# Kernel optimization log

Measured on AMD Instinct MI355X. Metric: run time of the kernel, lower is better.

## Reference

```python
import jax, jax.numpy as jnp
import numpy as np

IN_DIM = 1024
HID = 256
OUT_DIM = 1000
NUM_BINS = 51
BATCH = 2048
N_LEGAL = 200


def setup_inputs() -> dict:
    key = jax.random.key(0)
    ks = jax.random.split(key, 12)
    s = lambda fan_in: 1.0 / np.sqrt(fan_in)
    u = lambda k, shp, b: jax.random.uniform(k, shp, jnp.float32, -b, b)
    return {
        "x": jax.random.normal(ks[0], (BATCH, IN_DIM), jnp.float32),
        # weights stored as [in, out] (math-equivalent to torch Linear)
        "w_in": u(ks[1], (IN_DIM, HID), s(IN_DIM)),
        "b_in": u(ks[2], (HID,), s(IN_DIM)),
        "w_ah": u(ks[3], (HID, HID), s(HID)),
        "b_ah": u(ks[4], (HID,), s(HID)),
        "w_ao": u(ks[5], (HID, OUT_DIM * NUM_BINS), s(HID)),
        "b_ao": u(ks[6], (OUT_DIM * NUM_BINS,), s(HID)),
        "w_vh": u(ks[7], (HID, HID), s(HID)),
        "b_vh": u(ks[8], (HID,), s(HID)),
        "w_vo": u(ks[9], (HID, NUM_BINS), s(HID)),
        "b_vo": u(ks[10], (NUM_BINS,), s(HID)),
        "v_range": jnp.linspace(-10.0, 10.0, NUM_BINS, dtype=jnp.float32),
        "possible_moves": jax.random.randint(ks[11], (BATCH, N_LEGAL), 0, OUT_DIM),
    }


def reference(x, w_in, b_in, w_ah, b_ah, w_ao, b_ao, w_vh, b_vh, w_vo, b_vo,
              v_range, possible_moves):
    B = x.shape[0]
    h = jax.nn.relu(x @ w_in + b_in)                       # [B, 256]
    adv_h = jax.nn.relu(h @ w_ah + b_ah)                   # [B, 256]
    val_h = jax.nn.relu(h @ w_vh + b_vh)                   # [B, 256]
    adv = (adv_h @ w_ao + b_ao).reshape(B, OUT_DIM, NUM_BINS)
    val = (val_h @ w_vo + b_vo).reshape(B, 1, NUM_BINS)
    q = val + adv - adv.mean(axis=1, keepdims=True)        # [B, A, bins]
    p = jnp.maximum(jax.nn.softmax(q, axis=2), 1e-5)       # softmax + clamp(min=1e-5)
    q_vals = jnp.sum(p * v_range, axis=2)                  # [B, A]
    # LegalSoftmax: per-row scatter of 1.0 at legal indices, vectorized
    mask = jnp.zeros((B, OUT_DIM), x.dtype).at[
        jnp.arange(B)[:, None], possible_moves].set(1.0)
    filtered = q_vals * mask
    # faithful to torch: any exact-zero entry (masked OR coincidental) -> -inf
    return jnp.where(filtered == 0, -jnp.inf, filtered)
```

## Files before the change

### kernel.cpp

```cpp
#include <hip/hip_runtime.h>
#include <cstdint>
#include <cstddef>

#define NB      2048
#define INDIM   1024
#define HID     256
#define NA      1000
#define BINS    51
#define NLEG    200
#define NPAIR   (NB*NLEG)
#define NBLK    256
#define PPB     (NPAIR/NBLK)

#define NEG_SENTINEL (-1.0e30f)

typedef float    f32x4  __attribute__((ext_vector_type(4)));
typedef __bf16   bf16x8 __attribute__((ext_vector_type(8)));
typedef unsigned short us8 __attribute__((ext_vector_type(8)));
typedef unsigned short us4 __attribute__((ext_vector_type(4)));
typedef unsigned long long u64x2 __attribute__((ext_vector_type(2)));

__device__ __forceinline__ unsigned short f2bf(float f) {
  union { float f; unsigned u; } v; v.f = f;
  return (unsigned short)((v.u + 0x7FFFu + ((v.u >> 16) & 1u)) >> 16);
}
__device__ __forceinline__ float bf2f(unsigned short h) {
  union { unsigned u; float f; } v; v.u = ((unsigned)h) << 16;
  return v.f;
}
__device__ __forceinline__ bf16x8 as_bf(us8 v) { return __builtin_bit_cast(bf16x8, v); }
__device__ __forceinline__ int imin(int a, int b) { return a < b ? a : b; }

__device__ __forceinline__ unsigned f2fp8x4(float a, float b, float c, float d) {
  int v = 0;
  v = __builtin_amdgcn_cvt_pk_fp8_f32(a, b, v, false);
  v = __builtin_amdgcn_cvt_pk_fp8_f32(c, d, v, true);
  return (unsigned)v;
}
__device__ __forceinline__ unsigned char f2fp8(float f) {
  int v = __builtin_amdgcn_cvt_pk_fp8_f32(f, 0.f, 0, false);
  return (unsigned char)(v & 0xff);
}
__device__ __forceinline__ float fp82f(unsigned char u) {
  return __builtin_amdgcn_cvt_f32_fp8((int)u, 0);
}

__device__ __forceinline__ void pack_body(
    int s, int a0, char* smem, int tid,
    const float* __restrict__ w_ao, unsigned char* __restrict__ wp8,
    float* __restrict__ wmean_acc) {
  unsigned char* st = (unsigned char*)smem;
  const float* wbase = w_ao + (size_t)(s * 32) * (NA * BINS) + a0 * BINS;
  for (int i = tid; i < 32 * 102; i += 256) {
    int r = i / 102, c4 = i - r * 102;
    float4 f = *(const float4*)(wbase + (size_t)r * (NA * BINS) + c4 * 4);
    *(unsigned*)(st + r * 420 + c4 * 4) =
        f2fp8x4(f.x * 16.f, f.y * 16.f, f.z * 16.f, f.w * 16.f);
  }
  __syncthreads();
  for (int i = tid; i < 32 * 51; i += 256) {
    int r = i / 51, j = i - r * 51;
    float s8 = 0.f;
#pragma unroll
    for (int aL = 0; aL < 8; aL++) s8 += fp82f(st[r * 420 + aL * 51 + j]);
    atomicAdd(&wmean_acc[(size_t)(s * 32 + r) * BINS + j], s8);
  }
  int t4 = (tid >> 6) & 3, l = tid & 63;
  int col = t4 * 16 + (l & 15), kg = l >> 4;
  for (int aL = 0; aL < 8; aL++) {
    unsigned lo = 0, hi = 0;
    if (col < BINS) {
      const unsigned char* p0 = st + (kg * 8) * 420 + aL * 51 + col;
      lo = (unsigned)p0[0] | ((unsigned)p0[420] << 8) |
           ((unsigned)p0[840] << 16) | ((unsigned)p0[1260] << 24);
      hi = (unsigned)p0[1680] | ((unsigned)p0[2100] << 8) |
           ((unsigned)p0[2520] << 16) | ((unsigned)p0[2940] << 24);
    }
    uint2 v; v.x = lo; v.y = hi;
    *(uint2*)(wp8 + (size_t)(a0 + aL) * 16384 +
              (size_t)((s * 2 + (t4 >> 1)) * 64 + l) * 16 + (t4 & 1) * 8) = v;
  }
}

__global__ __launch_bounds__(256) void k_phase1(
    const float* __restrict__ w_ao, unsigned char* __restrict__ wp8,
    float* __restrict__ wmean_acc,
    const float* __restrict__ w_in, const float* __restrict__ w_ah,
    const float* __restrict__ w_vh,
    unsigned short* __restrict__ w_inT, unsigned short* __restrict__ w_ahT,
    unsigned short* __restrict__ w_vhT,
    float* __restrict__ out, const int* __restrict__ pm,
    int* __restrict__ cnt,
    const float* __restrict__ x, unsigned short* __restrict__ x_bf) {
  __shared__ __align__(16) char smem[13440];
  int b = blockIdx.x, tid = threadIdx.x;
  if (b < 500) {
    pack_body(b & 3, (b >> 2) * 8, smem, tid, w_ao, wp8, wmean_acc);
  } else if (b < 884) {
    int bb = b - 500;
    float (*tile)[33] = (float(*)[33])smem;
    const float* w; unsigned short* wT; int K, N, kt, nt;
    if (bb < 256)      { w = w_in; wT = w_inT; K = INDIM; N = HID; kt = bb & 31;        nt = bb >> 5; }
    else if (bb < 320) { w = w_ah; wT = w_ahT; K = HID;   N = HID; kt = (bb - 256) & 7; nt = (bb - 256) >> 3; }
    else               { w = w_vh; wT = w_vhT; K = HID;   N = HID; kt = (bb - 320) & 7; nt = (bb - 320) >> 3; }
    int k0 = kt * 32, n0 = nt * 32;
    int cr = tid >> 5, cc = tid & 31;
#pragma unroll
    for (int it = 0; it < 4; it++)
      tile[cr + it * 8][cc] = w[(size_t)(k0 + cr + it * 8) * N + n0 + cc];
    __syncthreads();
#pragma unroll
    for (int it = 0; it < 4; it++)
      wT[(size_t)(n0 + cr + it * 8) * K + k0 + cc] = f2bf(tile[cc][cr + it * 8]);
  } else if (b < 1384) {
    int base = (b - 884) * 1024 + tid;
    float4 v = {NEG_SENTINEL, NEG_SENTINEL, NEG_SENTINEL, NEG_SENTINEL};
#pragma unroll
    for (int it = 0; it < 4; it++) ((float4*)out)[base + it * 256] = v;
  } else if (b < 1640) {
    int* lh = (int*)smem;
    int blk = b - 1384;
    for (int i = tid; i < NA; i += 256) lh[i] = 0;
    __syncthreads();
    int base = blk * PPB;
    for (int i = tid; i < PPB; i += 256) atomicAdd(&lh[pm[base + i]], 1);
    __syncthreads();
    for (int a = tid; a < NA; a += 256) {
      int v = lh[a];
      if (v) atomicAdd(&cnt[a], v);
    }
  } else {
    int base4 = (b - 1640) * 1024 + tid;
#pragma unroll
    for (int it = 0; it < 4; it++) {
      float4 v = ((const float4*)x)[base4 + it * 256];
      us4 o;
      o[0] = f2bf(v.x); o[1] = f2bf(v.y); o[2] = f2bf(v.z); o[3] = f2bf(v.w);
      ((us4*)x_bf)[base4 + it * 256] = o;
    }
  }
}

__global__ __launch_bounds__(256) void k_phase2(
    const float* __restrict__ w_ao, unsigned char* __restrict__ wp8,
    float* __restrict__ wmean_acc,
    const int* __restrict__ cnt,
    const unsigned short* __restrict__ x_bf, const unsigned short* __restrict__ w_inT,
    const float* __restrict__ b_in, unsigned short* __restrict__ h_bf,
    int* __restrict__ off, int* __restrict__ cursor) {
  __shared__ __align__(16) char smem[13440];
  int b = blockIdx.x, tid = threadIdx.x;
  if (b < 500) {
    pack_body(4 + (b & 3), (b >> 2) * 8, smem, tid, w_ao, wp8, wmean_acc);
  } else if (b < 1012) {
    int w = tid >> 6, l = tid & 63, la = l & 15, g = l >> 4;
    int idx = (b - 500) * 4 + w;
    int m0 = (idx & 127) * 16, n0 = (idx >> 7) * 16;
    f32x4 acc = {0.f, 0.f, 0.f, 0.f};
    const us8* Bp = (const us8*)(w_inT + (size_t)(n0 + la) * INDIM) + g;
    const us8* Ap = (const us8*)(x_bf + (size_t)(m0 + la) * INDIM) + g;
#pragma unroll 8
    for (int s = 0; s < 32; s++)
      acc = __builtin_amdgcn_mfma_f32_16x16x32_bf16(as_bf(Ap[s * 4]), as_bf(Bp[s * 4]),
                                                    acc, 0, 0, 0);
    float bb = b_in[n0 + la];
#pragma unroll
    for (int r = 0; r < 4; r++) {
      float v = fmaxf(acc[r] + bb, 0.f);
      h_bf[(size_t)(m0 + g * 4 + r) * HID + n0 + la] = f2bf(v);
    }
  } else {
    int* s = (int*)smem;
    int t = tid, i0 = 4 * t;
    int v0 = (i0     < NA) ? cnt[i0]     : 0;
    int v1 = (i0 + 1 < NA) ? cnt[i0 + 1] : 0;
    int v2 = (i0 + 2 < NA) ? cnt[i0 + 2] : 0;
    int v3 = (i0 + 3 < NA) ? cnt[i0 + 3] : 0;
    int sum = v0 + v1 + v2 + v3;
    s[t] = sum;
    __syncthreads();
    for (int d = 1; d < 256; d <<= 1) {
      int u = (t >= d) ? s[t - d] : 0;
      __syncthreads();
      s[t] += u;
      __syncthreads();
    }
    int excl = s[t] - sum;
    if (i0     < NA) { off[i0]     = excl;                cursor[i0]     = excl; }
    if (i0 + 1 < NA) { off[i0 + 1] = excl + v0;           cursor[i0 + 1] = excl + v0; }
    if (i0 + 2 < NA) { off[i0 + 2] = excl + v0 + v1;      cursor[i0 + 2] = excl + v0 + v1; }
    if (i0 + 3 < NA) { off[i0 + 3] = excl + v0 + v1 + v2; cursor[i0 + 3] = excl + v0 + v1 + v2; }
  }
}

__global__ __launch_bounds__(256) void k_phase3(
    const unsigned short* __restrict__ h,
    const unsigned short* __restrict__ wA, const float* __restrict__ bA,
    unsigned char* __restrict__ Aext8, unsigned short* __restrict__ advh_bf,
    const unsigned short* __restrict__ wV, const float* __restrict__ bV,
    unsigned short* __restrict__ oV,
    const int* __restrict__ pm, int* __restrict__ cursor,
    int* __restrict__ rows,
    const float* __restrict__ w_vo, const float* __restrict__ wmean_acc,
    const float* __restrict__ b_vo, const float* __restrict__ b_ao,
    unsigned short* __restrict__ Wc, float* __restrict__ bias_c) {
  __shared__ int lc[NA];
  __shared__ int lbase[NA];
  __shared__ float sred[256];
  int b = blockIdx.x, tid = threadIdx.x;
  if (b < 1024) {
    int w = tid >> 6, l = tid & 63, la = l & 15, g = l >> 4;
    int idx = b * 4 + w;
    int m0 = (idx & 127) * 16;
    int ny = idx >> 7;
    int second = ny >> 4;
    int n0 = (ny & 15) * 16;
    const unsigned short* BT = second ? wV : wA;
    const float* bias = second ? bV : bA;
    f32x4 acc = {0.f, 0.f, 0.f, 0.f};
    const us8* Bp = (const us8*)(BT + (size_t)(n0 + la) * HID) + g;
    const us8* Ap = (const us8*)(h + (size_t)(m0 + la) * HID) + g;
#pragma unroll
    for (int s = 0; s < 8; s++)
      acc = __builtin_amdgcn_mfma_f32_16x16x32_bf16(as_bf(Ap[s * 4]), as_bf(Bp[s * 4]),
                                                    acc, 0, 0, 0);
    float bb = bias[n0 + la];
#pragma unroll
    for (int r = 0; r < 4; r++) {
      float v = fmaxf(acc[r] + bb, 0.f);
      size_t o = (size_t)(m0 + g * 4 + r) * HID + n0 + la;
      if (second) {
        oV[o] = f2bf(v);
      } else {
        advh_bf[o] = f2bf(v);
        Aext8[o] = f2fp8(v);
      }
    }
  } else if (b < 1280) {
    int blk = b - 1024, t = tid;
    for (int i = t; i < NA; i += 256) lc[i] = 0;
    __syncthreads();
    int pbase = blk * PPB;
    for (int i = t; i < PPB; i += 256) atomicAdd(&lc[pm[pbase + i]], 1);
    __syncthreads();
    for (int i = t; i < NA; i += 256) {
      int v = lc[i];
      lbase[i] = v ? atomicAdd(&cursor[i], v) : 0;
      lc[i] = 0;
    }
    __syncthreads();
    for (int i = t; i < PPB; i += 256) {
      int a = pm[pbase + i];
      int r = atomicAdd(&lc[a], 1);
      rows[lbase[a] + r] = (pbase + i) / NLEG;
    }
  } else {
    int n = b - 1280, t = tid;
    for (int k = t; k < 512; k += 256) {
      float v = 0.f;
      if (n < BINS)
        v = (k < 256) ? w_vo[(size_t)k * BINS + n]
                      : (-(0.001f / 16.f) * wmean_acc[(size_t)(k - 256) * BINS + n]);
      Wc[(size_t)n * 512 + k] = f2bf(v);
    }
    float acc = 0.f;
    if (n < BINS)
      for (int a = t; a < NA; a += 256) acc += b_ao[(size_t)a * BINS + n];
    sred[t] = acc;
    __syncthreads();
    for (int d = 128; d > 0; d >>= 1) { if (t < d) sred[t] += sred[t + d]; __syncthreads(); }
    if (t == 0) bias_c[n] = (n < BINS) ? (b_vo[n] - 0.001f * sred[0]) : 0.f;
  }
}

__global__ __launch_bounds__(256) void k_phase4(
    const unsigned short* __restrict__ valh, const unsigned short* __restrict__ advh,
    const unsigned short* __restrict__ Wc, const float* __restrict__ bias_c,
    float* __restrict__ cbuf_f) {
  int b = blockIdx.x, tid = threadIdx.x;
  int w = tid >> 6, l = tid & 63, la = l & 15, g = l >> 4;
  int idx = b * 4 + w;
  int m0 = (idx & 127) * 16;
  int n0 = ((idx >> 7) & 3) * 16;
  int half = idx >> 9;
  const unsigned short* A = half ? advh : valh;
  f32x4 acc = {0.f, 0.f, 0.f, 0.f};
  const us8* Bp = (const us8*)(Wc + (size_t)(n0 + la) * 512 + half * 256) + g;
  const us8* Ap = (const us8*)(A + (size_t)(m0 + la) * HID) + g;
#pragma unroll
  for (int s = 0; s < 8; s++)
    acc = __builtin_amdgcn_mfma_f32_16x16x32_bf16(as_bf(Ap[s * 4]), as_bf(Bp[s * 4]),
                                                  acc, 0, 0, 0);
  float bb = half ? 0.f : bias_c[n0 + la];
#pragma unroll
  for (int r = 0; r < 4; r++)
    atomicAdd(&cbuf_f[(size_t)(m0 + g * 4 + r) * 64 + n0 + la], acc[r] + bb);
}

#define TILE_BODY(TILE, RA_) do {                                              \
  int rA = (RA_);                                                              \
  const long long* Ap = (const long long*)(Aext8 + (size_t)rA * HID) + g;      \
  const float4* cf = (const float4*)(cbuf_f + (size_t)rA * 64);                \
  long long a8[8];                                                             \
  _Pragma("unroll") for (int s = 0; s < 8; s++) a8[s] = Ap[s * 4];             \
  float4 cq0 = cf[g], cq1 = cf[4 + g], cq2 = cf[8 + g], cq3 = cf[12 + g];      \
  f32x4 acc0 = {0.f,0.f,0.f,0.f}, acc1 = {0.f,0.f,0.f,0.f};                    \
  f32x4 acc2 = {0.f,0.f,0.f,0.f}, acc3 = {0.f,0.f,0.f,0.f};                    \
  __builtin_amdgcn_s_setprio(1);                                               \
  _Pragma("unroll") for (int s = 0; s < 8; s++) {                              \
    u64x2 b01 = sBv[(s * 2) * 64 + l];                                         \
    u64x2 b23 = sBv[(s * 2 + 1) * 64 + l];                                     \
    acc0 = __builtin_amdgcn_mfma_f32_16x16x32_fp8_fp8(                         \
        (long long)b01[0], a8[s], acc0, 0, 0, 0);                              \
    acc1 = __builtin_amdgcn_mfma_f32_16x16x32_fp8_fp8(                         \
        (long long)b01[1], a8[s], acc1, 0, 0, 0);                              \
    acc2 = __builtin_amdgcn_mfma_f32_16x16x32_fp8_fp8(                         \
        (long long)b23[0], a8[s], acc2, 0, 0, 0);                              \
    acc3 = __builtin_amdgcn_mfma_f32_16x16x32_fp8_fp8(                         \
        (long long)b23[1], a8[s], acc3, 0, 0, 0);                              \
  }                                                                            \
  __builtin_amdgcn_s_setprio(0);                                               \
  float S = 0.f;                                                               \
  f32x4 e0, e1, e2, e3;                                                        \
  _Pragma("unroll") for (int r = 0; r < 4; r++) {                              \
    e0[r] = __expf(fmaf(acc0[r], 0.0625f, cq0[r] + bao0[r])); S += e0[r];      \
    e1[r] = __expf(fmaf(acc1[r], 0.0625f, cq1[r] + bao1[r])); S += e1[r];      \
    e2[r] = __expf(fmaf(acc2[r], 0.0625f, cq2[r] + bao2[r])); S += e2[r];      \
    e3[r] = __expf(fmaf(acc3[r], 0.0625f, cq3[r] + bao3[r])); S += e3[r];      \
  }                                                                            \
  S += __shfl_xor(S, 16); S += __shfl_xor(S, 32);                              \
  float inv = 1.f / S, qv = 0.f;                                               \
  _Pragma("unroll") for (int r = 0; r < 4; r++) {                              \
    int bin = g * 4 + r;                                                       \
    qv = fmaf(fmaxf(e0[r] * inv, 1e-5f), (float)bin * 0.4f - 10.f, qv);        \
    qv = fmaf(fmaxf(e1[r] * inv, 1e-5f), (float)(bin + 16) * 0.4f - 10.f, qv); \
    qv = fmaf(fmaxf(e2[r] * inv, 1e-5f), (float)(bin + 32) * 0.4f - 10.f, qv); \
    if (bin + 48 < BINS)                                                       \
      qv = fmaf(fmaxf(e3[r] * inv, 1e-5f), (float)(bin + 48) * 0.4f - 10.f, qv); \
  }                                                                            \
  qv += __shfl_xor(qv, 16); qv += __shfl_xor(qv, 32);                          \
  int gi = (TILE) * 16 + la;                                                   \
  if (g == 0 && gi < count)                                                    \
    out[(size_t)rA * NA + a] = (qv == 0.f) ? NEG_SENTINEL : qv;                \
} while (0)

__global__ __launch_bounds__(256) void k_main_mfma(
    const unsigned char* __restrict__ Aext8,
    const float* __restrict__ cbuf_f,
    const unsigned char* __restrict__ wp8,
    const float* __restrict__ b_ao,
    const int* __restrict__ cnt, const int* __restrict__ off,
    const int* __restrict__ rows,
    float* __restrict__ out) {
  __shared__ __align__(16) long long sB8[2048];
  const u64x2* sBv = (const u64x2*)sB8;
  int bx = blockIdx.x;
  int a = (bx & 7) * 125 + (bx >> 3);
  int count = cnt[a];
  int ntiles = (count + 15) >> 4;
  if ((int)(blockIdx.y * 4) >= ntiles) return;
  int tid = threadIdx.x;
  int w = tid >> 6, l = tid & 63, la = l & 15, g = l >> 4;
  int base = off[a];
  int t0 = blockIdx.y * 4 + w;

  int rAq0 = rows[base + imin( t0       * 16 + la, count - 1)];
  int rAq1 = rows[base + imin((t0 +  8) * 16 + la, count - 1)];
  int rAq2 = rows[base + imin((t0 + 16) * 16 + la, count - 1)];
  int rAq3 = rows[base + imin((t0 + 24) * 16 + la, count - 1)];

  const float* baop = b_ao + (size_t)a * BINS;
  f32x4 bao0, bao1, bao2, bao3;
#pragma unroll
  for (int r = 0; r < 4; r++) {
    int bin = g * 4 + r;
    bao0[r] = baop[bin];
    bao1[r] = baop[bin + 16];
    bao2[r] = baop[bin + 32];
    bao3[r] = (bin + 48 < BINS) ? baop[bin + 48] : NEG_SENTINEL;
  }

  const u64x2* wpa = (const u64x2*)(wp8 + (size_t)a * 16384);
#pragma unroll
  for (int i = 0; i < 4; i++) ((u64x2*)sB8)[tid + i * 256] = wpa[tid + i * 256];
  __syncthreads();

  if (t0      < ntiles) TILE_BODY(t0,      rAq0);
  if (t0 +  8 < ntiles) TILE_BODY(t0 +  8, rAq1);
  if (t0 + 16 < ntiles) TILE_BODY(t0 + 16, rAq2);
  if (t0 + 24 < ntiles) TILE_BODY(t0 + 24, rAq3);
  for (int tile = t0 + 32; tile < ntiles; tile += 8) {
    int rAt = rows[base + imin(tile * 16 + la, count - 1)];
    TILE_BODY(tile, rAt);
  }
}

extern "C" void kernel_launch(void* const* d_in, const int* in_sizes, int n_in,
                              void* d_out, int out_size, void* d_ws, size_t ws_size,
                              hipStream_t stream) {
  (void)in_sizes; (void)n_in; (void)out_size; (void)ws_size;
  const float* x     = (const float*)d_in[0];
  const float* w_in  = (const float*)d_in[1];
  const float* b_in  = (const float*)d_in[2];
  const float* w_ah  = (const float*)d_in[3];
  const float* b_ah  = (const float*)d_in[4];
  const float* w_ao  = (const float*)d_in[5];
  const float* b_ao  = (const float*)d_in[6];
  const float* w_vh  = (const float*)d_in[7];
  const float* b_vh  = (const float*)d_in[8];
  const float* w_vo  = (const float*)d_in[9];
  const float* b_vo  = (const float*)d_in[10];
  const int*   pm    = (const int*)d_in[12];
  float* out = (float*)d_out;

  char* p = (char*)d_ws;
  unsigned char*  wp8     = (unsigned char*)p;  p += (size_t)NA * 32 * 512;
  unsigned char*  Aext8   = (unsigned char*)p;  p += (size_t)NB * HID;
  unsigned short* h_bf    = (unsigned short*)p; p += (size_t)NB * HID * 2;
  unsigned short* advh_bf = (unsigned short*)p; p += (size_t)NB * HID * 2;
  unsigned short* valh_bf = (unsigned short*)p; p += (size_t)NB * HID * 2;
  unsigned short* w_inT   = (unsigned short*)p; p += (size_t)HID * INDIM * 2;
  unsigned short* w_ahT   = (unsigned short*)p; p += (size_t)HID * HID * 2;
  unsigned short* w_vhT   = (unsigned short*)p; p += (size_t)HID * HID * 2;
  unsigned short* Wc      = (unsigned short*)p; p += (size_t)64 * 512 * 2;
  unsigned short* x_bf    = (unsigned short*)p; p += (size_t)NB * INDIM * 2;
  float* bias_c = (float*)p; p += 64 * 4;
  float* cbuf_f = (float*)p; p += (size_t)NB * 64 * 4;
  float* wmean  = (float*)p; p += 13056 * 4;
  int* cnt    = (int*)p; p += NA * 4;
  int* off    = (int*)p; p += NA * 4;
  int* cursor = (int*)p; p += (size_t)NA * 4 + 240;
  int* rows   = (int*)p; p += (size_t)NPAIR * 4 + 256;

  hipMemsetAsync(cbuf_f, 0, ((size_t)NB * 64 + 13056 + NA) * sizeof(float), stream);

  k_phase1<<<2152, 256, 0, stream>>>(w_ao, wp8, wmean, w_in, w_ah, w_vh,
                                     w_inT, w_ahT, w_vhT, out, pm, cnt,
                                     x, x_bf);
  k_phase2<<<1013, 256, 0, stream>>>(w_ao, wp8, wmean, cnt,
                                     x_bf, w_inT, b_in, h_bf, off, cursor);
  k_phase3<<<1344, 256, 0, stream>>>(h_bf, w_ahT, b_ah, Aext8, advh_bf,
                                     w_vhT, b_vh, valh_bf, pm, cursor, rows,
                                     w_vo, wmean, b_vo, b_ao, Wc, bias_c);
  k_phase4<<<256, 256, 0, stream>>>(valh_bf, advh_bf, Wc, bias_c, cbuf_f);
  k_main_mfma<<<dim3(1000, 2), 256, 0, stream>>>(Aext8, cbuf_f, wp8, b_ao,
                                                 cnt, off, rows, out);
}
```

Measured before the change: 209.7 us.

## Restructure pipeline into four kernels with fused heads and transposed fp8 packing

After: 209.6 us. No clear change (-0.0%).

```diff
diff --git a/kernel.cpp b/kernel.cpp
--- a/kernel.cpp
+++ b/kernel.cpp
@@ -24,10 +24,6 @@
   union { float f; unsigned u; } v; v.f = f;
   return (unsigned short)((v.u + 0x7FFFu + ((v.u >> 16) & 1u)) >> 16);
 }
-__device__ __forceinline__ float bf2f(unsigned short h) {
-  union { unsigned u; float f; } v; v.u = ((unsigned)h) << 16;
-  return v.f;
-}
 __device__ __forceinline__ bf16x8 as_bf(us8 v) { return __builtin_bit_cast(bf16x8, v); }
 __device__ __forceinline__ int imin(int a, int b) { return a < b ? a : b; }
 
@@ -45,44 +41,7 @@
   return __builtin_amdgcn_cvt_f32_fp8((int)u, 0);
 }
 
-__device__ __forceinline__ void pack_body(
-    int s, int a0, char* smem, int tid,
-    const float* __restrict__ w_ao, unsigned char* __restrict__ wp8,
-    float* __restrict__ wmean_acc) {
-  unsigned char* st = (unsigned char*)smem;
-  const float* wbase = w_ao + (size_t)(s * 32) * (NA * BINS) + a0 * BINS;
-  for (int i = tid; i < 32 * 102; i += 256) {
-    int r = i / 102, c4 = i - r * 102;
-    float4 f = *(const float4*)(wbase + (size_t)r * (NA * BINS) + c4 * 4);
-    *(unsigned*)(st + r * 420 + c4 * 4) =
-        f2fp8x4(f.x * 16.f, f.y * 16.f, f.z * 16.f, f.w * 16.f);
-  }
-  __syncthreads();
-  for (int i = tid; i < 32 * 51; i += 256) {
-    int r = i / 51, j = i - r * 51;
-    float s8 = 0.f;
-#pragma unroll
-    for (int aL = 0; aL < 8; aL++) s8 += fp82f(st[r * 420 + aL * 51 + j]);
-    atomicAdd(&wmean_acc[(size_t)(s * 32 + r) * BINS + j], s8);
-  }
-  int t4 = (tid >> 6) & 3, l = tid & 63;
-  int col = t4 * 16 + (l & 15), kg = l >> 4;
-  for (int aL = 0; aL < 8; aL++) {
-    unsigned lo = 0, hi = 0;
-    if (col < BINS) {
-      const unsigned char* p0 = st + (kg * 8) * 420 + aL * 51 + col;
-      lo = (unsigned)p0[0] | ((unsigned)p0[420] << 8) |
-           ((unsigned)p0[840] << 16) | ((unsigned)p0[1260] << 24);
-      hi = (unsigned)p0[1680] | ((unsigned)p0[2100] << 8) |
-           ((unsigned)p0[2520] << 16) | ((unsigned)p0[2940] << 24);
-    }
-    uint2 v; v.x = lo; v.y = hi;
-    *(uint2*)(wp8 + (size_t)(a0 + aL) * 16384 +
-              (size_t)((s * 2 + (t4 >> 1)) * 64 + l) * 16 + (t4 & 1) * 8) = v;
-  }
-}
-
-__global__ __launch_bounds__(256) void k_phase1(
+__global__ __launch_bounds__(256) void k_pre(
     const float* __restrict__ w_ao, unsigned char* __restrict__ wp8,
     float* __restrict__ wmean_acc,
     const float* __restrict__ w_in, const float* __restrict__ w_ah,
@@ -92,12 +51,67 @@
     float* __restrict__ out, const int* __restrict__ pm,
     int* __restrict__ cnt,
     const float* __restrict__ x, unsigned short* __restrict__ x_bf) {
-  __shared__ __align__(16) char smem[13440];
+  __shared__ __align__(16) unsigned char smem[16320];
   int b = blockIdx.x, tid = threadIdx.x;
-  if (b < 500) {
-    pack_body(b & 3, (b >> 2) * 8, smem, tid, w_ao, wp8, wmean_acc);
-  } else if (b < 884) {
-    int bb = b - 500;
+  if (b < 1000) {
+    unsigned char* st = smem;
+    int s = b & 7, a0 = (b >> 3) * 8;
+    const float* wbase = w_ao + (size_t)(s * 32) * (NA * BINS) + a0 * BINS;
+    for (int i = tid; i < 816; i += 256) {
+      int kq = i / 102, c4 = i - kq * 102;
+      const float* rp = wbase + (size_t)(kq * 4) * (NA * BINS) + c4 * 4;
+      float4 f0 = *(const float4*)(rp);
+      float4 f1 = *(const float4*)(rp + NA * BINS);
+      float4 f2 = *(const float4*)(rp + 2 * NA * BINS);
+      float4 f3 = *(const float4*)(rp + 3 * NA * BINS);
+      unsigned pk0 = f2fp8x4(f0.x * 16.f, f0.y * 16.f, f0.z * 16.f, f0.w * 16.f);
+      unsigned pk1 = f2fp8x4(f1.x * 16.f, f1.y * 16.f, f1.z * 16.f, f1.w * 16.f);
+      unsigned pk2 = f2fp8x4(f2.x * 16.f, f2.y * 16.f, f2.z * 16.f, f2.w * 16.f);
+      unsigned pk3 = f2fp8x4(f3.x * 16.f, f3.y * 16.f, f3.z * 16.f, f3.w * 16.f);
+      unsigned s01lo = __builtin_amdgcn_perm(pk1, pk0, 0x05010400u);
+      unsigned s01hi = __builtin_amdgcn_perm(pk1, pk0, 0x07030602u);
+      unsigned s23lo = __builtin_amdgcn_perm(pk3, pk2, 0x05010400u);
+      unsigned s23hi = __builtin_amdgcn_perm(pk3, pk2, 0x07030602u);
+      unsigned o0 = __builtin_amdgcn_perm(s23lo, s01lo, 0x05040100u);
+      unsigned o1 = __builtin_amdgcn_perm(s23lo, s01lo, 0x07060302u);
+      unsigned o2 = __builtin_amdgcn_perm(s23hi, s01hi, 0x05040100u);
+      unsigned o3 = __builtin_amdgcn_perm(s23hi, s01hi, 0x07060302u);
+      int k4 = kq * 4;
+      int swz = ((c4 >> 2) & 3) << 3;
+      int kb = ((k4 & 24) ^ swz) + (k4 & 7);
+      int cbase = c4 * 160;
+      *(unsigned*)(st + cbase + kb)       = o0;
+      *(unsigned*)(st + cbase + 40 + kb)  = o1;
+      *(unsigned*)(st + cbase + 80 + kb)  = o2;
+      *(unsigned*)(st + cbase + 120 + kb) = o3;
+    }
+    __syncthreads();
+    for (int i = tid; i < 32 * 51; i += 256) {
+      int r = i / 51, j = i - r * 51;
+      float s8 = 0.f;
+#pragma unroll
+      for (int aL = 0; aL < 8; aL++) {
+        int c = aL * 51 + j;
+        s8 += fp82f(st[c * 40 + ((r & 24) ^ (((c >> 4) & 3) << 3)) + (r & 7)]);
+      }
+      atomicAdd(&wmean_acc[(size_t)(s * 32 + r) * BINS + j], s8);
+    }
+    int t4 = (tid >> 6) & 3, l = tid & 63;
+    int col = t4 * 16 + (l & 15), kg = l >> 4;
+    for (int aL = 0; aL < 8; aL++) {
+      unsigned lo = 0, hi = 0;
+      if (col < BINS) {
+        int ci = aL * 51 + col;
+        unsigned long long v8 = *(const unsigned long long*)(
+            st + ci * 40 + ((kg * 8) ^ (((ci >> 4) & 3) << 3)));
+        lo = (unsigned)v8; hi = (unsigned)(v8 >> 32);
+      }
+      uint2 v; v.x = lo; v.y = hi;
+      *(uint2*)(wp8 + (size_t)(a0 + aL) * 16384 +
+                (size_t)((s * 2 + (t4 >> 1)) * 64 + l) * 16 + (t4 & 1) * 8) = v;
+    }
+  } else if (b < 1384) {
+    int bb = b - 1000;
     float (*tile)[33] = (float(*)[33])smem;
     const float* w; unsigned short* wT; int K, N, kt, nt;
     if (bb < 256)      { w = w_in; wT = w_inT; K = INDIM; N = HID; kt = bb & 31;        nt = bb >> 5; }
@@ -112,25 +126,13 @@
 #pragma unroll
     for (int it = 0; it < 4; it++)
       wT[(size_t)(n0 + cr + it * 8) * K + k0 + cc] = f2bf(tile[cc][cr + it * 8]);
-  } else if (b < 1384) {
-    int base = (b - 884) * 1024 + tid;
+  } else if (b < 1884) {
+    int base = (b - 1384) * 1024 + tid;
     float4 v = {NEG_SENTINEL, NEG_SENTINEL, NEG_SENTINEL, NEG_SENTINEL};
 #pragma unroll
     for (int it = 0; it < 4; it++) ((float4*)out)[base + it * 256] = v;
-  } else if (b < 1640) {
-    int* lh = (int*)smem;
-    int blk = b - 1384;
-    for (int i = tid; i < NA; i += 256) lh[i] = 0;
-    __syncthreads();
-    int base = blk * PPB;
-    for (int i = tid; i < PPB; i += 256) atomicAdd(&lh[pm[base + i]], 1);
-    __syncthreads();
-    for (int a = tid; a < NA; a += 256) {
-      int v = lh[a];
-      if (v) atomicAdd(&cnt[a], v);
-    }
-  } else {
-    int base4 = (b - 1640) * 1024 + tid;
+  } else if (b < 2396) {
+    int base4 = (b - 1884) * 1024 + tid;
 #pragma unroll
     for (int it = 0; it < 4; it++) {
       float4 v = ((const float4*)x)[base4 + it * 256];
@@ -138,23 +140,33 @@
       o[0] = f2bf(v.x); o[1] = f2bf(v.y); o[2] = f2bf(v.z); o[3] = f2bf(v.w);
       ((us4*)x_bf)[base4 + it * 256] = o;
     }
+  } else {
+    int* lh = (int*)smem;
+    int blk = b - 2396;
+    for (int i = tid; i < NA; i += 256) lh[i] = 0;
+    __syncthreads();
+    int base = blk * PPB;
+    for (int i = tid; i < PPB; i += 256) atomicAdd(&lh[pm[base + i]], 1);
+    __syncthreads();
+    for (int a = tid; a < NA; a += 256) {
+      int v = lh[a];
+      if (v) atomicAdd(&cnt[a], v);
+    }
   }
 }
 
-__global__ __launch_bounds__(256) void k_phase2(
-    const float* __restrict__ w_ao, unsigned char* __restrict__ wp8,
-    float* __restrict__ wmean_acc,
-    const int* __restrict__ cnt,
+__global__ __launch_bounds__(256) void k_mid(
     const unsigned short* __restrict__ x_bf, const unsigned short* __restrict__ w_inT,
     const float* __restrict__ b_in, unsigned short* __restrict__ h_bf,
-    int* __restrict__ off, int* __restrict__ cursor) {
-  __shared__ __align__(16) char smem[13440];
+    const float* __restrict__ w_vo, const float* __restrict__ wmean_acc,
+    const float* __restrict__ b_vo, const float* __restrict__ b_ao,
+    unsigned short* __restrict__ Wc, float* __restrict__ bias_c,
+    const int* __restrict__ cnt, int* __restrict__ off, int* __restrict__ cursor) {
+  __shared__ __align__(16) char smem[1024];
   int b = blockIdx.x, tid = threadIdx.x;
-  if (b < 500) {
-    pack_body(4 + (b & 3), (b >> 2) * 8, smem, tid, w_ao, wp8, wmean_acc);
-  } else if (b < 1012) {
+  if (b < 512) {
     int w = tid >> 6, l = tid & 63, la = l & 15, g = l >> 4;
-    int idx = (b - 500) * 4 + w;
+    int idx = b * 4 + w;
     int m0 = (idx & 127) * 16, n0 = (idx >> 7) * 16;
     f32x4 acc = {0.f, 0.f, 0.f, 0.f};
     const us8* Bp = (const us8*)(w_inT + (size_t)(n0 + la) * INDIM) + g;
@@ -169,6 +181,23 @@
       float v = fmaxf(acc[r] + bb, 0.f);
       h_bf[(size_t)(m0 + g * 4 + r) * HID + n0 + la] = f2bf(v);
     }
+  } else if (b < 576) {
+    float* sred = (float*)smem;
+    int n = b - 512, t = tid;
+    for (int k = t; k < 512; k += 256) {
+      float v = 0.f;
+      if (n < BINS)
+        v = (k < 256) ? w_vo[(size_t)k * BINS + n]
+                      : (-(0.001f / 16.f) * wmean_acc[(size_t)(k - 256) * BINS + n]);
+      Wc[(size_t)n * 512 + k] = f2bf(v);
+    }
+    float acc = 0.f;
+    if (n < BINS)
+      for (int a = t; a < NA; a += 256) acc += b_ao[(size_t)a * BINS + n];
+    sred[t] = acc;
+    __syncthreads();
+    for (int d = 128; d > 0; d >>= 1) { if (t < d) sred[t] += sred[t + d]; __syncthreads(); }
+    if (t == 0) bias_c[n] = (n < BINS) ? (b_vo[n] - 0.001f * sred[0]) : 0.f;
   } else {
     int* s = (int*)smem;
     int t = tid, i0 = 4 * t;
@@ -193,51 +222,71 @@
   }
 }
 
-__global__ __launch_bounds__(256) void k_phase3(
+__global__ __launch_bounds__(256) void k_heads(
     const unsigned short* __restrict__ h,
     const unsigned short* __restrict__ wA, const float* __restrict__ bA,
-    unsigned char* __restrict__ Aext8, unsigned short* __restrict__ advh_bf,
     const unsigned short* __restrict__ wV, const float* __restrict__ bV,
-    unsigned short* __restrict__ oV,
-    const int* __restrict__ pm, int* __restrict__ cursor,
-    int* __restrict__ rows,
-    const float* __restrict__ w_vo, const float* __restrict__ wmean_acc,
-    const float* __restrict__ b_vo, const float* __restrict__ b_ao,
-    unsigned short* __restrict__ Wc, float* __restrict__ bias_c) {
-  __shared__ int lc[NA];
-  __shared__ int lbase[NA];
-  __shared__ float sred[256];
+    const unsigned short* __restrict__ Wc, const float* __restrict__ bias_c,
+    unsigned char* __restrict__ Aext8, float* __restrict__ cbuf_f,
+    const int* __restrict__ pm, int* __restrict__ cursor, int* __restrict__ rows) {
+  __shared__ __align__(16) char smem[16896];
   int b = blockIdx.x, tid = threadIdx.x;
-  if (b < 1024) {
+  if (b < 128) {
+    unsigned short* aL = (unsigned short*)smem;
+    unsigned short* vL = (unsigned short*)smem + 16 * 264;
     int w = tid >> 6, l = tid & 63, la = l & 15, g = l >> 4;
-    int idx = b * 4 + w;
-    int m0 = (idx & 127) * 16;
-    int ny = idx >> 7;
-    int second = ny >> 4;
-    int n0 = (ny & 15) * 16;
-    const unsigned short* BT = second ? wV : wA;
-    const float* bias = second ? bV : bA;
+    int m0 = b * 16;
+    const us8* Ap = (const us8*)(h + (size_t)(m0 + la) * HID) + g;
+    us8 aF[8];
+#pragma unroll
+    for (int s = 0; s < 8; s++) aF[s] = Ap[s * 4];
+#pragma unroll
+    for (int part = 0; part < 2; part++) {
+      const unsigned short* BT = part ? wV : wA;
+      const float* bias = part ? bV : bA;
+      unsigned short* oL = part ? vL : aL;
+#pragma unroll
+      for (int nt = 0; nt < 4; nt++) {
+        int n0 = w * 64 + nt * 16;
+        f32x4 acc = {0.f, 0.f, 0.f, 0.f};
+        const us8* Bp = (const us8*)(BT + (size_t)(n0 + la) * HID) + g;
+#pragma unroll
+        for (int s = 0; s < 8; s++)
+          acc = __builtin_amdgcn_mfma_f32_16x16x32_bf16(as_bf(aF[s]), as_bf(Bp[s * 4]),
+                                                        acc, 0, 0, 0);
+        float bb = bias[n0 + la];
+#pragma unroll
+        for (int r = 0; r < 4; r++) {
+          float v = fmaxf(acc[r] + bb, 0.f);
+          oL[(g * 4 + r) * 264 + n0 + la] = f2bf(v);
+          if (part == 0)
+            Aext8[(size_t)(m0 + g * 4 + r) * HID + n0 + la] = f2fp8(v);
+        }
+      }
+    }
+    __syncthreads();
+    int n0c = w * 16;
     f32x4 acc = {0.f, 0.f, 0.f, 0.f};
-    const us8* Bp = (const us8*)(BT + (size_t)(n0 + la) * HID) + g;
-    const us8* Ap = (const us8*)(h + (size_t)(m0 + la) * HID) + g;
+    const us8* Vp  = (const us8*)(vL + la * 264) + g;
+    const us8* Ap2 = (const us8*)(aL + la * 264) + g;
+    const us8* BpV = (const us8*)(Wc + (size_t)(n0c + la) * 512) + g;
+    const us8* BpA = (const us8*)(Wc + (size_t)(n0c + la) * 512 + 256) + g;
 #pragma unroll
     for (int s = 0; s < 8; s++)
-      acc = __builtin_amdgcn_mfma_f32_16x16x32_bf16(as_bf(Ap[s * 4]), as_bf(Bp[s * 4]),
+      acc = __builtin_amdgcn_mfma_f32_16x16x32_bf16(as_bf(Vp[s * 4]), as_bf(BpV[s * 4]),
                                                     acc, 0, 0, 0);
-    float bb = bias[n0 + la];
-#pragma unroll
-    for (int r = 0; r < 4; r++) {
-      float v = fmaxf(acc[r] + bb, 0.f);
-      size_t o = (size_t)(m0 + g * 4 + r) * HID + n0 + la;
-      if (second) {
-        oV[o] = f2bf(v);
-      } else {
-        advh_bf[o] = f2bf(v);
-        Aext8[o] = f2fp8(v);
-      }
-    }
-  } else if (b < 1280) {
-    int blk = b - 1024, t = tid;
+#pragma unroll
+    for (int s = 0; s < 8; s++)
+      acc = __builtin_amdgcn_mfma_f32_16x16x32_bf16(as_bf(Ap2[s * 4]), as_bf(BpA[s * 4]),
+                                                    acc, 0, 0, 0);
+    float bb = bias_c[n0c + la];
+#pragma unroll
+    for (int r = 0; r < 4; r++)
+      cbuf_f[(size_t)(m0 + g * 4 + r) * 64 + n0c + la] = acc[r] + bb;
+  } else {
+    int* lc = (int*)smem;
+    int* lbase = (int*)(smem + 4096);
+    int blk = b - 128, t = tid;
     for (int i = t; i < NA; i += 256) lc[i] = 0;
     __syncthreads();
     int pbase = blk * PPB;
@@ -254,47 +303,7 @@
       int r = atomicAdd(&lc[a], 1);
       rows[lbase[a] + r] = (pbase + i) / NLEG;
     }
-  } else {
-    int n = b - 1280, t = tid;
-    for (int k = t; k < 512; k += 256) {
-      float v = 0.f;
-      if (n < BINS)
-        v = (k < 256) ? w_vo[(size_t)k * BINS + n]
-                      : (-(0.001f / 16.f) * wmean_acc[(size_t)(k - 256) * BINS + n]);
-      Wc[(size_t)n * 512 + k] = f2bf(v);
-    }
-    float acc = 0.f;
-    if (n < BINS)
-      for (int a = t; a < NA; a += 256) acc += b_ao[(size_t)a * BINS + n];
-    sred[t] = acc;
-    __syncthreads();
-    for (int d = 128; d > 0; d >>= 1) { if (t < d) sred[t] += sred[t + d]; __syncthreads(); }
-    if (t == 0) bias_c[n] = (n < BINS) ? (b_vo[n] - 0.001f * sred[0]) : 0.f;
   }
-}
-
-__global__ __launch_bounds__(256) void k_phase4(
-    const unsigned short* __restrict__ valh, const unsigned short* __restrict__ advh,
-    const unsigned short* __restrict__ Wc, const float* __restrict__ bias_c,
-    float* __restrict__ cbuf_f) {
-  int b = blockIdx.x, tid = threadIdx.x;
-  int w = tid >> 6, l = tid & 63, la = l & 15, g = l >> 4;
-  int idx = b * 4 + w;
-  int m0 = (idx & 127) * 16;
-  int n0 = ((idx >> 7) & 3) * 16;
-  int half = idx >> 9;
-  const unsigned short* A = half ? advh : valh;
-  f32x4 acc = {0.f, 0.f, 0.f, 0.f};
-  const us8* Bp = (const us8*)(Wc + (size_t)(n0 + la) * 512 + half * 256) + g;
-  const us8* Ap = (const us8*)(A + (size_t)(m0 + la) * HID) + g;
-#pragma unroll
-  for (int s = 0; s < 8; s++)
-    acc = __builtin_amdgcn_mfma_f32_16x16x32_bf16(as_bf(Ap[s * 4]), as_bf(Bp[s * 4]),
-                                                  acc, 0, 0, 0);
-  float bb = half ? 0.f : bias_c[n0 + la];
-#pragma unroll
-  for (int r = 0; r < 4; r++)
-    atomicAdd(&cbuf_f[(size_t)(m0 + g * 4 + r) * 64 + n0 + la], acc[r] + bb);
 }
 
 #define TILE_BODY(TILE, RA_) do {                                              \
@@ -364,10 +373,8 @@
   int base = off[a];
   int t0 = blockIdx.y * 4 + w;
 
-  int rAq0 = rows[base + imin( t0       * 16 + la, count - 1)];
-  int rAq1 = rows[base + imin((t0 +  8) * 16 + la, count - 1)];
-  int rAq2 = rows[base + imin((t0 + 16) * 16 + la, count - 1)];
-  int rAq3 = rows[base + imin((t0 + 24) * 16 + la, count - 1)];
+  int rQ0 = rows[base + imin( t0       * 16 + la, count - 1)];
+  int rQ1 = rows[base + imin((t0 + 16) * 16 + la, count - 1)];
 
   const float* baop = b_ao + (size_t)a * BINS;
   f32x4 bao0, bao1, bao2, bao3;
@@ -385,11 +392,9 @@
   for (int i = 0; i < 4; i++) ((u64x2*)sB8)[tid + i * 256] = wpa[tid + i * 256];
   __syncthreads();
 
-  if (t0      < ntiles) TILE_BODY(t0,      rAq0);
-  if (t0 +  8 < ntiles) TILE_BODY(t0 +  8, rAq1);
-  if (t0 + 16 < ntiles) TILE_BODY(t0 + 16, rAq2);
-  if (t0 + 24 < ntiles) TILE_BODY(t0 + 24, rAq3);
-  for (int tile = t0 + 32; tile < ntiles; tile += 8) {
+  if (t0      < ntiles) TILE_BODY(t0,      rQ0);
+  if (t0 + 16 < ntiles) TILE_BODY(t0 + 16, rQ1);
+  for (int tile = t0 + 32; tile < ntiles; tile += 16) {
     int rAt = rows[base + imin(tile * 16 + la, count - 1)];
     TILE_BODY(tile, rAt);
   }
@@ -417,8 +422,6 @@
   unsigned char*  wp8     = (unsigned char*)p;  p += (size_t)NA * 32 * 512;
   unsigned char*  Aext8   = (unsigned char*)p;  p += (size_t)NB * HID;
   unsigned short* h_bf    = (unsigned short*)p; p += (size_t)NB * HID * 2;
-  unsigned short* advh_bf = (unsigned short*)p; p += (size_t)NB * HID * 2;
-  unsigned short* valh_bf = (unsigned short*)p; p += (size_t)NB * HID * 2;
   unsigned short* w_inT   = (unsigned short*)p; p += (size_t)HID * INDIM * 2;
   unsigned short* w_ahT   = (unsigned short*)p; p += (size_t)HID * HID * 2;
   unsigned short* w_vhT   = (unsigned short*)p; p += (size_t)HID * HID * 2;
@@ -432,17 +435,16 @@
   int* cursor = (int*)p; p += (size_t)NA * 4 + 240;
   int* rows   = (int*)p; p += (size_t)NPAIR * 4 + 256;
 
-  hipMemsetAsync(cbuf_f, 0, ((size_t)NB * 64 + 13056 + NA) * sizeof(float), stream);
-
-  k_phase1<<<2152, 256, 0, stream>>>(w_ao, wp8, wmean, w_in, w_ah, w_vh,
-                                     w_inT, w_ahT, w_vhT, out, pm, cnt,
-                                     x, x_bf);
-  k_phase2<<<1013, 256, 0, stream>>>(w_ao, wp8, wmean, cnt,
-                                     x_bf, w_inT, b_in, h_bf, off, cursor);
-  k_phase3<<<1344, 256, 0, stream>>>(h_bf, w_ahT, b_ah, Aext8, advh_bf,
-                                     w_vhT, b_vh, valh_bf, pm, cursor, rows,
-                                     w_vo, wmean, b_vo, b_ao, Wc, bias_c);
-  k_phase4<<<256, 256, 0, stream>>>(valh_bf, advh_bf, Wc, bias_c, cbuf_f);
-  k_main_mfma<<<dim3(1000, 2), 256, 0, stream>>>(Aext8, cbuf_f, wp8, b_ao,
+  hipMemsetAsync(wmean, 0, (13056 + NA) * sizeof(float), stream);
+
+  k_pre<<<2652, 256, 0, stream>>>(w_ao, wp8, wmean, w_in, w_ah, w_vh,
+                                  w_inT, w_ahT, w_vhT, out, pm, cnt, x, x_bf);
+  k_mid<<<577, 256, 0, stream>>>(x_bf, w_inT, b_in, h_bf,
+                                 w_vo, wmean, b_vo, b_ao, Wc, bias_c,
+                                 cnt, off, cursor);
+  k_heads<<<384, 256, 0, stream>>>(h_bf, w_ahT, b_ah, w_vhT, b_vh,
+                                   Wc, bias_c, Aext8, cbuf_f,
+                                   pm, cursor, rows);
+  k_main_mfma<<<dim3(1000, 4), 256, 0, stream>>>(Aext8, cbuf_f, wp8, b_ao,
                                                  cnt, off, rows, out);
 }
```
